# Performance work log

Hardware: AMD Instinct MI355X
Metric: run time of the kernel (lower is better)

The kernel has to match this reference:

```python
import jax, jax.numpy as jnp
import numpy as np

V, E, H, L, B = 32000, 128, 32, 64, 32


def setup_inputs() -> dict:
    key = jax.random.key(0)
    k0, k1, k2, k3, k4, k5 = jax.random.split(key, 6)
    stdv = 1.0 / np.sqrt(H)
    we = jax.random.uniform(k0, (V, E), minval=-stdv, maxval=stdv, dtype=jnp.float32)
    we = we.at[1].set(0.0)  # pad token row zeroed, as in original
    i2h1 = jax.random.uniform(k1, (E + H, H), minval=-stdv, maxval=stdv, dtype=jnp.float32)
    i2h2 = jax.random.uniform(k2, (E + H, H), minval=-stdv, maxval=stdv, dtype=jnp.float32)
    h2o = jax.random.uniform(k3, (2 * H, V), minval=-stdv, maxval=stdv, dtype=jnp.float32)
    bias = jnp.ones((1, H), dtype=jnp.float32)  # assigned after reset_parameters -> stays ones
    hidden_init = jax.random.normal(k4, (1, H), dtype=jnp.float32)  # plain buffer, not reset
    inp = jax.random.randint(k5, (L, B), 0, V, dtype=jnp.int64)
    return {"inp": inp, "we": we, "i2h1": i2h1, "i2h2": i2h2,
            "h2o": h2o, "bias": bias, "hidden_init": hidden_init}


def reference(inp, we, i2h1, i2h2, h2o, bias, hidden_init):
    Lr, Br = inp.shape
    Hh = hidden_init.shape[1]
    emb = we[inp]                                   # [L,B,E] embedding gather
    h0 = jnp.broadcast_to(hidden_init, (Br, Hh))    # [B,H]
    b = jnp.broadcast_to(bias, (Br, Hh))            # [B,H]

    def make_step(W):
        def step(h, e):
            h_new = jnp.tanh(jnp.concatenate([e, h], axis=1) @ W + b)
            return h_new, h_new
        return step

    # forward direction: hf[i] = hidden after consuming token i
    _, hf = jax.lax.scan(make_step(i2h1), h0, emb)
    # backward direction (scan over reversed time, flip back)
    _, hb_rev = jax.lax.scan(make_step(i2h2), h0, emb[::-1])
    hb = hb_rev[::-1]                               # hb[i] = bwd hidden after token i

    # original uses hiddenf[i] (pre-token-i fwd state) and hiddenb[i+1] (post-token-(i+1) bwd state)
    hf_used = jnp.concatenate([h0[None], hf[:-1]], axis=0)   # [L,B,H]
    hb_used = jnp.concatenate([hb[1:], h0[None]], axis=0)    # [L,B,H]

    hcat = jnp.concatenate([hf_used, hb_used], axis=-1)      # [L,B,2H]
    logits = jnp.einsum('lbh,hv->lbv', hcat, h2o)            # [L,B,V]
    return jax.nn.log_softmax(logits, axis=-1)
```

## Files before the change

### kernel.cpp

```cpp
#include <hip/hip_runtime.h>

#define V_SZ 32000
#define E_SZ 128
#define H_SZ 32
#define L_SZ 64
#define B_SZ 32
#define M_TOT 2048
#define K2 64
#define NVT 125
#define NPART 500

typedef __bf16 bf16x8 __attribute__((ext_vector_type(8)));
typedef float f32x4 __attribute__((ext_vector_type(4)));

__device__ __forceinline__ unsigned short f2bf(float f) {
    unsigned int u = __float_as_uint(f);
    u += 0x7FFFu + ((u >> 16) & 1u);
    return (unsigned short)(u >> 16);
}

__device__ __forceinline__ void load_vfrag(
    const __bf16* __restrict__ h2oT, int vbase, int lg, int lr,
    bf16x8 vf[4][2]) {
#pragma unroll
    for (int i = 0; i < 4; ++i) {
        const __bf16* vp = h2oT + (size_t)(vbase + i * 16 + lr) * K2 + lg * 8;
        vf[i][0] = *(const bf16x8*)(vp);
        vf[i][1] = *(const bf16x8*)(vp + 32);
    }
}

__device__ __forceinline__ void load_hfrag(
    const __bf16* __restrict__ hcat, int rowbase, int lg, int lr,
    bf16x8 hf[4][2]) {
#pragma unroll
    for (int j = 0; j < 4; ++j) {
        const __bf16* hp = hcat + (size_t)(rowbase + j * 16 + lr) * K2 + lg * 8;
        hf[j][0] = *(const bf16x8*)(hp);
        hf[j][1] = *(const bf16x8*)(hp + 32);
    }
}

__device__ __forceinline__ void tile_gemm_t(
    const bf16x8 vf[4][2], const bf16x8 hf[4][2], f32x4 acc[4][4]) {
#pragma unroll
    for (int i = 0; i < 4; ++i)
#pragma unroll
        for (int j = 0; j < 4; ++j) acc[i][j] = (f32x4){0.f, 0.f, 0.f, 0.f};
#pragma unroll
    for (int i = 0; i < 4; ++i)
#pragma unroll
        for (int j = 0; j < 4; ++j) {
            acc[i][j] = __builtin_amdgcn_mfma_f32_16x16x32_bf16(vf[i][0], hf[j][0], acc[i][j], 0, 0, 0);
            acc[i][j] = __builtin_amdgcn_mfma_f32_16x16x32_bf16(vf[i][1], hf[j][1], acc[i][j], 0, 0, 0);
        }
}

__global__ __launch_bounds__(256) void k_prep_rnn(
    const int* __restrict__ inp, const float* __restrict__ we,
    const float* __restrict__ i2h1, const float* __restrict__ i2h2,
    const float* __restrict__ h2o, const float* __restrict__ bias,
    const float* __restrict__ hinit,
    unsigned short* __restrict__ hcat_u, unsigned short* __restrict__ h2oT_u) {
    const int tid = threadIdx.x;
    const int p = blockIdx.x;
    if (p < 500) {
        const int v = p * 64 + (tid & 63);
        const int kg = tid >> 6;
        unsigned int* dst = (unsigned int*)(h2oT_u + (size_t)v * K2 + kg * 16);
#pragma unroll
        for (int kk = 0; kk < 16; kk += 2) {
            const int k = kg * 16 + kk;
            float a = h2o[(size_t)k * V_SZ + v];
            float b = h2o[(size_t)(k + 1) * V_SZ + v];
            dst[kk >> 1] = (unsigned int)f2bf(a) | ((unsigned int)f2bf(b) << 16);
        }
        return;
    }
    const int w2 = p - 500;
    const int dir = w2 >> 4;
    const int bpair = w2 & 15;
    const float* W = dir ? i2h2 : i2h1;
    __shared__ float Xl[L_SZ * 2 * H_SZ];
    {
        const int j = tid & 31, bb = (tid >> 5) & 1, to = tid >> 6;
        const int b = bpair * 2 + bb;
        const float bj = bias[j];
        for (int tt = 0; tt < 16; ++tt) {
            const int t = to * 16 + tt;
            const int idx = inp[t * B_SZ + b];
            const float* er = we + (size_t)idx * E_SZ;
            float acc = bj;
#pragma unroll
            for (int k0 = 0; k0 < E_SZ; k0 += 4) {
                f32x4 e4 = *(const f32x4*)(er + k0);
                acc += e4.x * W[(k0 + 0) * H_SZ + j];
                acc += e4.y * W[(k0 + 1) * H_SZ + j];
                acc += e4.z * W[(k0 + 2) * H_SZ + j];
                acc += e4.w * W[(k0 + 3) * H_SZ + j];
            }
            Xl[(t * 2 + bb) * H_SZ + j] = acc;
        }
    }
    __syncthreads();
    if (tid < 64) {
        const int lane = tid;
        const int bb = lane >> 5;
        const int b = bpair * 2 + bb;
        const int j = lane & 31;
        const int srcbase = lane & 32;
        float wh[H_SZ];
#pragma unroll
        for (int k = 0; k < H_SZ; ++k) wh[k] = W[(E_SZ + k) * H_SZ + j];
        float h = hinit[j];
        for (int step = 0; step < L_SZ; ++step) {
            const int tt = dir ? (L_SZ - 1 - step) : step;
            hcat_u[(tt * B_SZ + b) * K2 + dir * H_SZ + j] = f2bf(h);
            float a0 = Xl[(tt * 2 + bb) * H_SZ + j];
            float a1 = 0.f, a2 = 0.f, a3 = 0.f;
#pragma unroll
            for (int k = 0; k < H_SZ; k += 4) {
                a0 += __shfl(h, srcbase | k, 64) * wh[k];
                a1 += __shfl(h, srcbase | (k + 1), 64) * wh[k + 1];
                a2 += __shfl(h, srcbase | (k + 2), 64) * wh[k + 2];
                a3 += __shfl(h, srcbase | (k + 3), 64) * wh[k + 3];
            }
            float x2 = (a0 + a1) + (a2 + a3);
            float e = __expf(2.f * x2);
            h = 1.f - 2.f * __builtin_amdgcn_rcpf(e + 1.f);
        }
    }
}

__global__ __launch_bounds__(256) void k_pass_a(
    const __bf16* __restrict__ hcat, const __bf16* __restrict__ h2oT,
    float* __restrict__ Asum) {
    const int tid = threadIdx.x;
    const int wave = tid >> 6, lane = tid & 63;
    const int lg = lane >> 4, lr = lane & 15;
    const int y0 = blockIdx.y * 512;
    const int vbase = blockIdx.x * 256 + wave * 64;
    const int pcol = blockIdx.x * 4 + wave;

    bf16x8 vf[4][2];
    load_vfrag(h2oT, vbase, lg, lr, vf);

    auto epilogue = [&](const bf16x8 hf[4][2], int rowbase) {
        f32x4 acc[4][4];
        tile_gemm_t(vf, hf, acc);
        float srow[4];
#pragma unroll
        for (int j = 0; j < 4; ++j) {
            float s = 0.f;
#pragma unroll
            for (int i = 0; i < 4; ++i)
#pragma unroll
                for (int r = 0; r < 4; ++r) s += __expf(acc[i][j][r]);
            srow[j] = s;
        }
#pragma unroll
        for (int j = 0; j < 4; ++j) {
            srow[j] += __shfl_xor(srow[j], 16, 64);
            srow[j] += __shfl_xor(srow[j], 32, 64);
        }
        if (lane < 16) {
#pragma unroll
            for (int j = 0; j < 4; ++j)
                Asum[(size_t)pcol * M_TOT + rowbase + j * 16 + lane] = srow[j];
        }
    };

    bf16x8 hfA[4][2], hfB[4][2];
    load_hfrag(hcat, y0, lg, lr, hfA);
#pragma unroll
    for (int t = 0; t < 8; ++t) {
        if (t & 1) {
            if (t < 7) load_hfrag(hcat, y0 + (t + 1) * 64, lg, lr, hfA);
            epilogue(hfB, y0 + t * 64);
        } else {
            if (t < 7) load_hfrag(hcat, y0 + (t + 1) * 64, lg, lr, hfB);
            epilogue(hfA, y0 + t * 64);
        }
    }
}

__global__ __launch_bounds__(256) void k_lse(
    const float* __restrict__ Asum, float* __restrict__ lse) {
    const int row = blockIdx.x * 256 + threadIdx.x;
    float s = 0.f;
    for (int i = 0; i < NPART; ++i) s += Asum[(size_t)i * M_TOT + row];
    lse[row] = logf(s);
}

__global__ __launch_bounds__(256) void k_pass_b(
    const __bf16* __restrict__ hcat, const __bf16* __restrict__ h2oT,
    const float* __restrict__ lse, float* __restrict__ out) {
    const int tid = threadIdx.x;
    const int wave = tid >> 6, lane = tid & 63;
    const int lg = lane >> 4, lr = lane & 15;
    const int y0 = blockIdx.y * 512;
    const int vbase = blockIdx.x * 256 + wave * 64;

    bf16x8 vf[4][2];
    load_vfrag(h2oT, vbase, lg, lr, vf);

    auto epilogue = [&](const bf16x8 hf[4][2], int rowbase) {
        float lsev[4];
#pragma unroll
        for (int j = 0; j < 4; ++j)
            lsev[j] = lse[rowbase + j * 16 + lr];
        f32x4 acc[4][4];
        tile_gemm_t(vf, hf, acc);
#pragma unroll
        for (int j = 0; j < 4; ++j) {
            float* rp = out + (size_t)(rowbase + j * 16 + lr) * V_SZ + vbase + lg * 4;
#pragma unroll
            for (int i = 0; i < 4; ++i) {
                f32x4 v;
                v.x = acc[i][j].x - lsev[j];
                v.y = acc[i][j].y - lsev[j];
                v.z = acc[i][j].z - lsev[j];
                v.w = acc[i][j].w - lsev[j];
                *(f32x4*)(rp + i * 16) = v;
            }
        }
    };

    bf16x8 hfA[4][2], hfB[4][2];
    load_hfrag(hcat, y0, lg, lr, hfA);
#pragma unroll
    for (int t = 0; t < 8; ++t) {
        if (t & 1) {
            if (t < 7) load_hfrag(hcat, y0 + (t + 1) * 64, lg, lr, hfA);
            epilogue(hfB, y0 + t * 64);
        } else {
            if (t < 7) load_hfrag(hcat, y0 + (t + 1) * 64, lg, lr, hfB);
            epilogue(hfA, y0 + t * 64);
        }
    }
}

extern "C" void kernel_launch(void* const* d_in, const int* in_sizes, int n_in,
                              void* d_out, int out_size, void* d_ws, size_t ws_size,
                              hipStream_t stream) {
    (void)in_sizes; (void)n_in; (void)out_size; (void)ws_size;
    const int*   inp   = (const int*)d_in[0];
    const float* we    = (const float*)d_in[1];
    const float* i2h1  = (const float*)d_in[2];
    const float* i2h2  = (const float*)d_in[3];
    const float* h2o   = (const float*)d_in[4];
    const float* bias  = (const float*)d_in[5];
    const float* hinit = (const float*)d_in[6];
    float* out = (float*)d_out;
    char* ws = (char*)d_ws;
    unsigned short* hcat_u = (unsigned short*)(ws);
    unsigned short* h2oT_u = (unsigned short*)(ws + 262144);
    float*          Asum   = (float*)(ws + 4358144);
    float*          lse    = (float*)(ws + 8454144);

    k_prep_rnn<<<532, 256, 0, stream>>>(inp, we, i2h1, i2h2, h2o, bias, hinit,
                                        hcat_u, h2oT_u);
    k_pass_a<<<dim3(NVT, 4), 256, 0, stream>>>(
        (const __bf16*)hcat_u, (const __bf16*)h2oT_u, Asum);
    k_lse<<<8, 256, 0, stream>>>(Asum, lse);
    k_pass_b<<<dim3(NVT, 4), 256, 0, stream>>>(
        (const __bf16*)hcat_u, (const __bf16*)h2oT_u, lse, out);
}
```

Baseline: 158.3 us.

## Fuse softmax passes into cooperative kernel with atomic row sums

Replaces the per-partition sum buffer and separate reduction kernel with atomicAdd into a single per-row sum array, which is zeroed in the prep kernel. The two GEMM passes are merged into one cooperative kernel that keeps the vocab fragments in registers and uses a grid-wide sync between the exp-sum pass and the output pass. This removes two kernel launches, the reduction kernel and one reload of the vocab fragments. In exchange it adds atomic contention on 2048 rows and a grid barrier, and falls back to the two separate passes if a cooperative launch is not possible.

```diff
diff --git a/kernel.cpp b/kernel.cpp
--- a/kernel.cpp
+++ b/kernel.cpp
@@ -1,4 +1,7 @@
 #include <hip/hip_runtime.h>
+#include <hip/hip_cooperative_groups.h>
+
+namespace cg = cooperative_groups;
 
 #define V_SZ 32000
 #define E_SZ 128
@@ -8,7 +11,6 @@
 #define M_TOT 2048
 #define K2 64
 #define NVT 125
-#define NPART 500
 
 typedef __bf16 bf16x8 __attribute__((ext_vector_type(8)));
 typedef float f32x4 __attribute__((ext_vector_type(4)));
@@ -55,16 +57,96 @@
             acc[i][j] = __builtin_amdgcn_mfma_f32_16x16x32_bf16(vf[i][1], hf[j][1], acc[i][j], 0, 0, 0);
         }
 }
+
+template <typename EP>
+__device__ __forceinline__ void sweep8(
+    const __bf16* __restrict__ hcat, int y0, int lg, int lr, EP&& ep) {
+    bf16x8 hfA[4][2], hfB[4][2];
+    load_hfrag(hcat, y0, lg, lr, hfA);
+#pragma unroll
+    for (int t = 0; t < 8; ++t) {
+        if (t & 1) {
+            if (t < 7) load_hfrag(hcat, y0 + (t + 1) * 64, lg, lr, hfA);
+            ep(hfB, y0 + t * 64);
+        } else {
+            if (t < 7) load_hfrag(hcat, y0 + (t + 1) * 64, lg, lr, hfB);
+            ep(hfA, y0 + t * 64);
+        }
+    }
+}
+
+struct EpA {
+    const bf16x8 (*vf)[2];
+    float* S;
+    int lane, lg, lr;
+    __device__ __forceinline__ void operator()(const bf16x8 hf[4][2], int rowbase) const {
+        f32x4 acc[4][4];
+        tile_gemm_t((const bf16x8(*)[2])vf, hf, acc);
+        float srow[4];
+#pragma unroll
+        for (int j = 0; j < 4; ++j) {
+            float s = 0.f;
+#pragma unroll
+            for (int i = 0; i < 4; ++i)
+#pragma unroll
+                for (int r = 0; r < 4; ++r) s += __expf(acc[i][j][r]);
+            srow[j] = s;
+        }
+#pragma unroll
+        for (int j = 0; j < 4; ++j) {
+            srow[j] += __shfl_xor(srow[j], 16, 64);
+            srow[j] += __shfl_xor(srow[j], 32, 64);
+        }
+        if (lane < 16) {
+#pragma unroll
+            for (int j = 0; j < 4; ++j)
+                atomicAdd(&S[rowbase + j * 16 + lane], srow[j]);
+        }
+    }
+};
+
+struct EpB {
+    const bf16x8 (*vf)[2];
+    const float* S;
+    float* out;
+    int vbase, lg, lr;
+    __device__ __forceinline__ void operator()(const bf16x8 hf[4][2], int rowbase) const {
+        float lsev[4];
+#pragma unroll
+        for (int j = 0; j < 4; ++j)
+            lsev[j] = logf(S[rowbase + j * 16 + lr]);
+        f32x4 acc[4][4];
+        tile_gemm_t((const bf16x8(*)[2])vf, hf, acc);
+#pragma unroll
+        for (int j = 0; j < 4; ++j) {
+            float* rp = out + (size_t)(rowbase + j * 16 + lr) * V_SZ + vbase + lg * 4;
+#pragma unroll
+            for (int i = 0; i < 4; ++i) {
+                f32x4 v;
+                v.x = acc[i][j].x - lsev[j];
+                v.y = acc[i][j].y - lsev[j];
+                v.z = acc[i][j].z - lsev[j];
+                v.w = acc[i][j].w - lsev[j];
+                *(f32x4*)(rp + i * 16) = v;
+            }
+        }
+    }
+};
 
 __global__ __launch_bounds__(256) void k_prep_rnn(
     const int* __restrict__ inp, const float* __restrict__ we,
     const float* __restrict__ i2h1, const float* __restrict__ i2h2,
     const float* __restrict__ h2o, const float* __restrict__ bias,
     const float* __restrict__ hinit,
-    unsigned short* __restrict__ hcat_u, unsigned short* __restrict__ h2oT_u) {
+    unsigned short* __restrict__ hcat_u, unsigned short* __restrict__ h2oT_u,
+    float* __restrict__ S) {
     const int tid = threadIdx.x;
     const int p = blockIdx.x;
     if (p < 500) {
+        if (p == 0) {
+#pragma unroll
+            for (int i = tid; i < M_TOT; i += 256) S[i] = 0.f;
+        }
         const int v = p * 64 + (tid & 63);
         const int kg = tid >> 6;
         unsigned int* dst = (unsigned int*)(h2oT_u + (size_t)v * K2 + kg * 16);
@@ -132,112 +214,59 @@
     }
 }
 
+__global__ __launch_bounds__(256) void k_fused(
+    const unsigned short* __restrict__ hcat_u,
+    const unsigned short* __restrict__ h2oT_u,
+    float* __restrict__ S, float* __restrict__ out) {
+    cg::grid_group gg = cg::this_grid();
+    const int tid = threadIdx.x;
+    const int wave = tid >> 6, lane = tid & 63;
+    const int lg = lane >> 4, lr = lane & 15;
+    const int xcol = blockIdx.x >> 2;
+    const int y0 = (blockIdx.x & 3) * 512;
+    const int vbase = xcol * 256 + wave * 64;
+    const __bf16* hcat = (const __bf16*)hcat_u;
+    const __bf16* h2oT = (const __bf16*)h2oT_u;
+
+    bf16x8 vf[4][2];
+    load_vfrag(h2oT, vbase, lg, lr, vf);
+
+    EpA epa{vf, S, lane, lg, lr};
+    sweep8(hcat, y0, lg, lr, epa);
+
+    __threadfence();
+    gg.sync();
+
+    EpB epb{vf, S, out, vbase, lg, lr};
+    sweep8(hcat, y0, lg, lr, epb);
+}
+
 __global__ __launch_bounds__(256) void k_pass_a(
     const __bf16* __restrict__ hcat, const __bf16* __restrict__ h2oT,
-    float* __restrict__ Asum) {
+    float* __restrict__ S) {
     const int tid = threadIdx.x;
     const int wave = tid >> 6, lane = tid & 63;
     const int lg = lane >> 4, lr = lane & 15;
     const int y0 = blockIdx.y * 512;
     const int vbase = blockIdx.x * 256 + wave * 64;
-    const int pcol = blockIdx.x * 4 + wave;
-
     bf16x8 vf[4][2];
     load_vfrag(h2oT, vbase, lg, lr, vf);
-
-    auto epilogue = [&](const bf16x8 hf[4][2], int rowbase) {
-        f32x4 acc[4][4];
-        tile_gemm_t(vf, hf, acc);
-        float srow[4];
-#pragma unroll
-        for (int j = 0; j < 4; ++j) {
-            float s = 0.f;
-#pragma unroll
-            for (int i = 0; i < 4; ++i)
-#pragma unroll
-                for (int r = 0; r < 4; ++r) s += __expf(acc[i][j][r]);
-            srow[j] = s;
-        }
-#pragma unroll
-        for (int j = 0; j < 4; ++j) {
-            srow[j] += __shfl_xor(srow[j], 16, 64);
-            srow[j] += __shfl_xor(srow[j], 32, 64);
-        }
-        if (lane < 16) {
-#pragma unroll
-            for (int j = 0; j < 4; ++j)
-                Asum[(size_t)pcol * M_TOT + rowbase + j * 16 + lane] = srow[j];
-        }
-    };
-
-    bf16x8 hfA[4][2], hfB[4][2];
-    load_hfrag(hcat, y0, lg, lr, hfA);
-#pragma unroll
-    for (int t = 0; t < 8; ++t) {
-        if (t & 1) {
-            if (t < 7) load_hfrag(hcat, y0 + (t + 1) * 64, lg, lr, hfA);
-            epilogue(hfB, y0 + t * 64);
-        } else {
-            if (t < 7) load_hfrag(hcat, y0 + (t + 1) * 64, lg, lr, hfB);
-            epilogue(hfA, y0 + t * 64);
-        }
-    }
-}
-
-__global__ __launch_bounds__(256) void k_lse(
-    const float* __restrict__ Asum, float* __restrict__ lse) {
-    const int row = blockIdx.x * 256 + threadIdx.x;
-    float s = 0.f;
-    for (int i = 0; i < NPART; ++i) s += Asum[(size_t)i * M_TOT + row];
-    lse[row] = logf(s);
+    EpA epa{vf, S, lane, lg, lr};
+    sweep8(hcat, y0, lg, lr, epa);
 }
 
 __global__ __launch_bounds__(256) void k_pass_b(
     const __bf16* __restrict__ hcat, const __bf16* __restrict__ h2oT,
-    const float* __restrict__ lse, float* __restrict__ out) {
+    const float* __restrict__ S, float* __restrict__ out) {
     const int tid = threadIdx.x;
     const int wave = tid >> 6, lane = tid & 63;
     const int lg = lane >> 4, lr = lane & 15;
     const int y0 = blockIdx.y * 512;
     const int vbase = blockIdx.x * 256 + wave * 64;
-
     bf16x8 vf[4][2];
     load_vfrag(h2oT, vbase, lg, lr, vf);
-
-    auto epilogue = [&](const bf16x8 hf[4][2], int rowbase) {
-        float lsev[4];
-#pragma unroll
-        for (int j = 0; j < 4; ++j)
-            lsev[j] = lse[rowbase + j * 16 + lr];
-        f32x4 acc[4][4];
-        tile_gemm_t(vf, hf, acc);
-#pragma unroll
-        for (int j = 0; j < 4; ++j) {
-            float* rp = out + (size_t)(rowbase + j * 16 + lr) * V_SZ + vbase + lg * 4;
-#pragma unroll
-            for (int i = 0; i < 4; ++i) {
-                f32x4 v;
-                v.x = acc[i][j].x - lsev[j];
-                v.y = acc[i][j].y - lsev[j];
-                v.z = acc[i][j].z - lsev[j];
-                v.w = acc[i][j].w - lsev[j];
-                *(f32x4*)(rp + i * 16) = v;
-            }
-        }
-    };
-
-    bf16x8 hfA[4][2], hfB[4][2];
-    load_hfrag(hcat, y0, lg, lr, hfA);
-#pragma unroll
-    for (int t = 0; t < 8; ++t) {
-        if (t & 1) {
-            if (t < 7) load_hfrag(hcat, y0 + (t + 1) * 64, lg, lr, hfA);
-            epilogue(hfB, y0 + t * 64);
-        } else {
-            if (t < 7) load_hfrag(hcat, y0 + (t + 1) * 64, lg, lr, hfB);
-            epilogue(hfA, y0 + t * 64);
-        }
-    }
+    EpB epb{vf, S, out, vbase, lg, lr};
+    sweep8(hcat, y0, lg, lr, epb);
 }
 
 extern "C" void kernel_launch(void* const* d_in, const int* in_sizes, int n_in,
@@ -255,14 +284,23 @@
     char* ws = (char*)d_ws;
     unsigned short* hcat_u = (unsigned short*)(ws);
     unsigned short* h2oT_u = (unsigned short*)(ws + 262144);
-    float*          Asum   = (float*)(ws + 4358144);
-    float*          lse    = (float*)(ws + 8454144);
+    float*          S      = (float*)(ws + 4358144);
 
     k_prep_rnn<<<532, 256, 0, stream>>>(inp, we, i2h1, i2h2, h2o, bias, hinit,
-                                        hcat_u, h2oT_u);
-    k_pass_a<<<dim3(NVT, 4), 256, 0, stream>>>(
-        (const __bf16*)hcat_u, (const __bf16*)h2oT_u, Asum);
-    k_lse<<<8, 256, 0, stream>>>(Asum, lse);
-    k_pass_b<<<dim3(NVT, 4), 256, 0, stream>>>(
-        (const __bf16*)hcat_u, (const __bf16*)h2oT_u, lse, out);
-}
+                                        hcat_u, h2oT_u, S);
+
+    hipError_t e = hipErrorUnknown;
+    int occ = 0;
+    if (hipOccupancyMaxActiveBlocksPerMultiprocessor(&occ, k_fused, 256, 0)
+            == hipSuccess && occ * 256 >= 500) {
+        void* args[] = {(void*)&hcat_u, (void*)&h2oT_u, (void*)&S, (void*)&out};
+        e = hipLaunchCooperativeKernel((void*)k_fused, dim3(500), dim3(256),
+                                       args, 0, stream);
+    }
+    if (e != hipSuccess) {
+        k_pass_a<<<dim3(NVT, 4), 256, 0, stream>>>(
+            (const __bf16*)hcat_u, (const __bf16*)h2oT_u, S);
+        k_pass_b<<<dim3(NVT, 4), 256, 0, stream>>>(
+            (const __bf16*)hcat_u, (const __bf16*)h2oT_u, S, out);
+    }
+}
```

Measured after the change: 154.1 us. 2.7% less time.
